# Performance work log

Hardware: AMD Instinct MI355X
Metric: run time of the kernel (lower is better)

## Reference

```python
import jax, jax.numpy as jnp
import numpy as np

B, NPQ, NPV, NSL, K, ED, H = 64, 1024, 256, 1, 128, 16, 8
DK = K // H  # per-head dim (k_dim = v_dim = emb_dim // num_heads)
ETYPES = [("PQ","PQ"),("PQ","PV"),("PQ","Slack"),("PV","PQ"),("PV","PV"),("PV","Slack"),("Slack","PQ"),("Slack","PV")]
ECOUNTS = [262144, 131072, 4096, 131072, 65536, 2048, 4096, 2048]
NN = {"PQ": B*NPQ, "PV": B*NPV, "Slack": B*NSL}
LN_EPS = 1e-5


def setup_inputs() -> dict:
    ks = iter(jax.random.split(jax.random.key(0), 64))
    inp = {}
    for name, n in [("x_PQ", NN["PQ"]), ("x_PV", NN["PV"]), ("x_Slack", NN["Slack"])]:
        inp[name] = jax.random.normal(next(ks), (n, K), jnp.float32)
    for t, ((s, d), E) in enumerate(zip(ETYPES, ECOUNTS)):
        src = jax.random.randint(next(ks), (E,), 0, NN[s])
        dst = jax.random.randint(next(ks), (E,), 0, NN[d])
        inp[f"ei_{t}"] = jnp.stack([src, dst]).astype(jnp.int32)
        inp[f"ea_{t}"] = jax.random.normal(next(ks), (E, ED), jnp.float32)
    sc = 1.0 / np.sqrt(K)
    shapes = {"Wk": (2,8,K,K), "bk": (2,8,K), "Wq": (2,8,K,K), "bq": (2,8,K),
              "Wv": (2,8,K,K), "bv": (2,8,K), "Ws": (2,8,K,K), "bconv": (2,8,K),
              "We": (2,8,ED,K), "be": (2,8,K), "Wgt": (K,K), "bgt": (K,),
              "Wq1": (K,K), "Wk2": (K,K), "Wv2": (K,K), "Wo": (K,K), "bo": (K,)}
    for name, sh in shapes.items():
        inp[name] = jax.random.normal(next(ks), sh, jnp.float32) * sc
    inp["ln_g"] = jnp.ones((K,), jnp.float32)
    inp["ln_b"] = jnp.zeros((K,), jnp.float32)
    return inp


def _cross_attention(x1, x2, Wq1, Wk2, Wv2, Wo, bo):
    # x1: [B, N1, K] queries; x2: [B, N2, K] keys/values
    Bq, N1, _ = x1.shape
    N2 = x2.shape[1]
    q = (x1 @ Wq1).reshape(Bq, N1, H, DK)
    k = (x2 @ Wk2).reshape(Bq, N2, H, DK)
    v = (x2 @ Wv2).reshape(Bq, N2, H, DK)
    attn = jnp.einsum("bnhd,bmhd->bhnm", q, k) / np.sqrt(DK).astype(np.float32)
    attn = jax.nn.softmax(attn, axis=-1)
    out = jnp.einsum("bhnm,bmhd->bnhd", attn, v).reshape(Bq, N1, H * DK)
    return out @ Wo + bo


def _forward(x_PQ, x_PV, x_Slack, ei, ea,
             Wk, bk, Wq, bq, Wv, bv, Ws, bconv, We, be,
             Wgt, bgt, Wq1, Wk2, Wv2, Wo, bo, ln_g, ln_b):
    x = {"PQ": x_PQ, "PV": x_PV, "Slack": x_Slack}
    # global feature from input node features
    gf = jnp.concatenate([x_PQ.reshape(B, NPQ, K),
                          x_PV.reshape(B, NPV, K),
                          x_Slack.reshape(B, NSL, K)], axis=1)
    gf = gf @ Wgt + bgt
    gnode = jnp.concatenate([gf.mean(axis=1, keepdims=True),
                             gf.max(axis=1, keepdims=True)], axis=1)  # [B, 2, K]
    # 2 HeteroConv layers of ResGatedGraphConv, aggr='sum' over edge types
    for l in range(2):
        new = {t: jnp.zeros((NN[t], K), x_PQ.dtype) for t in ("PQ", "PV", "Slack")}
        for t, (s, d) in enumerate(ETYPES):
            xs, xd = x[s], x[d]
            k_ = xd @ Wk[l, t] + bk[l, t]   # lin_key on dst
            q_ = xs @ Wq[l, t] + bq[l, t]   # lin_query on src
            v_ = xs @ Wv[l, t] + bv[l, t]   # lin_value on src
            e_ = ea[t] @ We[l, t] + be[l, t]  # lin_edge
            si, di = ei[t][0], ei[t][1]
            gate = jax.nn.sigmoid(k_[di] + q_[si] + e_)  # [E, K]
            agg = jax.ops.segment_sum(gate * v_[si], di, num_segments=NN[d])
            new[d] = new[d] + agg + xd @ Ws[l, t] + bconv[l, t]
        x = {t: jax.nn.relu(v) for t, v in new.items()}
    # cross-attention vs. global mean/max nodes, residual, layernorm (PQ, PV only)
    res = {}
    for key2, N1 in (("PQ", NPQ), ("PV", NPV)):
        x1 = x[key2].reshape(B, N1, K)
        ca = _cross_attention(x1, gnode, Wq1, Wk2, Wv2, Wo, bo).reshape(B * N1, K)
        h = x[key2] + ca
        mu = h.mean(axis=-1, keepdims=True)
        var = ((h - mu) ** 2).mean(axis=-1, keepdims=True)
        res[key2] = (h - mu) * jax.lax.rsqrt(var + LN_EPS) * ln_g + ln_b
    return res["PQ"], res["PV"], x["Slack"]


def reference(x_PQ, x_PV, x_Slack,
              ei_0, ei_1, ei_2, ei_3, ei_4, ei_5, ei_6, ei_7,
              ea_0, ea_1, ea_2, ea_3, ea_4, ea_5, ea_6, ea_7,
              Wk, bk, Wq, bq, Wv, bv, Ws, bconv, We, be,
              Wgt, bgt, Wq1, Wk2, Wv2, Wo, bo, ln_g, ln_b):
    ei = [ei_0, ei_1, ei_2, ei_3, ei_4, ei_5, ei_6, ei_7]
    ea = [ea_0, ea_1, ea_2, ea_3, ea_4, ea_5, ea_6, ea_7]
    return _forward(x_PQ, x_PV, x_Slack, ei, ea,
                    Wk, bk, Wq, bq, Wv, bv, Ws, bconv, We, be,
                    Wgt, bgt, Wq1, Wk2, Wv2, Wo, bo, ln_g, ln_b)
```

## Files before the change

kernel.cpp:

```cpp
#include <hip/hip_runtime.h>
#include <hip/hip_bf16.h>
#include <math.h>

#define N_PQ 65536
#define N_PV 16384
#define N_SL 64

typedef __attribute__((ext_vector_type(8))) short s16x8;
typedef __attribute__((ext_vector_type(4))) float f32x4;

__device__ __forceinline__ ushort f2bf(float f) {
    union { float f; unsigned u; } x; x.f = f;
    unsigned r = x.u + 0x7fff + ((x.u >> 16) & 1);
    return (ushort)(r >> 16);
}
__device__ __forceinline__ float bf2f(ushort u) {
    union { unsigned u; float f; } x; x.u = ((unsigned)u) << 16;
    return x.f;
}

template<int OUT_BF16>
__global__ __launch_bounds__(256) void gemm_mfma(
    const ushort* __restrict__ A, const ushort* __restrict__ Bt,
    const float* __restrict__ bias, void* __restrict__ Cv, int M, int N)
{
    __shared__ ushort As[128 * 128];
    const int tid = threadIdx.x;
    const int m0 = blockIdx.x * 128;
    const int n0 = blockIdx.y * 128;

    #pragma unroll
    for (int p = 0; p < 8; ++p) {
        int c = p * 256 + tid;
        int row = c >> 4, c16 = c & 15;
        int gr = m0 + row;
        int4 v = make_int4(0, 0, 0, 0);
        if (gr < M) v = *(const int4*)(A + (size_t)gr * 128 + c16 * 8);
        *(int4*)(As + row * 128 + (c16 ^ (row & 7)) * 8) = v;
    }
    __syncthreads();

    const int lane = tid & 63, wave = tid >> 6;
    const int wr = wave >> 1, wc = wave & 1;
    const int lrow = lane & 15, lk = lane >> 4;

    f32x4 acc[4][4];
    #pragma unroll
    for (int mi = 0; mi < 4; ++mi)
        #pragma unroll
        for (int ni = 0; ni < 4; ++ni) acc[mi][ni] = (f32x4){0.f, 0.f, 0.f, 0.f};

    #pragma unroll
    for (int kk = 0; kk < 4; ++kk) {
        s16x8 a[4], b[4];
        #pragma unroll
        for (int mi = 0; mi < 4; ++mi) {
            int row = wr * 64 + mi * 16 + lrow;
            int c16 = (lk + kk * 4) ^ (row & 7);
            a[mi] = *(const s16x8*)(As + row * 128 + c16 * 8);
        }
        #pragma unroll
        for (int ni = 0; ni < 4; ++ni) {
            int n = n0 + wc * 64 + ni * 16 + lrow;
            b[ni] = *(const s16x8*)(Bt + (size_t)n * 128 + kk * 32 + lk * 8);
        }
        #pragma unroll
        for (int mi = 0; mi < 4; ++mi)
            #pragma unroll
            for (int ni = 0; ni < 4; ++ni)
                acc[mi][ni] = __builtin_amdgcn_mfma_f32_16x16x32_bf16(
                    a[mi], b[ni], acc[mi][ni], 0, 0, 0);
    }

    if (OUT_BF16) {
        __syncthreads();
        ushort* Cl = As;
        #pragma unroll
        for (int mi = 0; mi < 4; ++mi)
            #pragma unroll
            for (int ni = 0; ni < 4; ++ni)
                #pragma unroll
                for (int r = 0; r < 4; ++r) {
                    int row = wr * 64 + mi * 16 + (lane >> 4) * 4 + r;
                    int col = wc * 64 + ni * 16 + (lane & 15);
                    float v = acc[mi][ni][r] + (bias ? bias[n0 + col] : 0.f);
                    Cl[row * 128 + (((col >> 3) ^ (row & 7)) << 3) + (col & 7)] = f2bf(v);
                }
        __syncthreads();
        ushort* C = (ushort*)Cv;
        #pragma unroll
        for (int p = 0; p < 8; ++p) {
            int c = p * 256 + tid;
            int row = c >> 4, c16 = c & 15;
            int gr = m0 + row;
            if (gr < M)
                *(int4*)(C + (size_t)gr * N + n0 + c16 * 8) =
                    *(const int4*)(As + row * 128 + (c16 ^ (row & 7)) * 8);
        }
    } else {
        float* C = (float*)Cv;
        #pragma unroll
        for (int mi = 0; mi < 4; ++mi)
            #pragma unroll
            for (int ni = 0; ni < 4; ++ni)
                #pragma unroll
                for (int r = 0; r < 4; ++r) {
                    int row = m0 + wr * 64 + mi * 16 + (lane >> 4) * 4 + r;
                    int col = n0 + wc * 64 + ni * 16 + (lane & 15);
                    if (row < M)
                        C[(size_t)row * N + col] =
                            acc[mi][ni][r] + (bias ? bias[col] : 0.f);
                }
    }
}

__global__ void prep_mats(
    const float* __restrict__ Wk, const float* __restrict__ Wq,
    const float* __restrict__ Wv, const float* __restrict__ Ws,
    const float* __restrict__ Wgt, const float* __restrict__ Wq1,
    const float* __restrict__ Wk2, const float* __restrict__ Wv2,
    const float* __restrict__ Wo,
    ushort* __restrict__ panels, ushort* __restrict__ wssum,
    ushort* __restrict__ finalw)
{
    const int m = blockIdx.x >> 6;
    const int e = (blockIdx.x & 63) * 256 + threadIdx.x;
    const int nl = e >> 7, k = e & 127;
    const int dstlist[3][3] = {{0,3,6},{1,4,7},{2,5,-1}};
    const int srclist[3][3] = {{0,1,2},{3,4,5},{6,7,-1}};
    const int nkg[3] = {3,3,2};
    const int gofs[3] = {0,1280,2560};

    if (m < 52) {
        int l = m / 26, r = m % 26;
        int g, slot;
        if (r < 10)      { g = 0; slot = r; }
        else if (r < 20) { g = 1; slot = r - 10; }
        else             { g = 2; slot = r - 20; }
        int nk = nkg[g];
        float val; int col;
        if (slot < nk) {
            int t = dstlist[g][slot];
            val = Wk[(size_t)(l * 8 + t) * 16384 + k * 128 + nl];
            col = slot * 128 + nl;
        } else if (slot < 2 * nk) {
            int s = slot - nk; int t = srclist[g][s];
            val = Wq[(size_t)(l * 8 + t) * 16384 + k * 128 + nl];
            col = nk * 128 + s * 256 + ((nl >> 1) << 2) + (nl & 1);
        } else if (slot < 3 * nk) {
            int s = slot - 2 * nk; int t = srclist[g][s];
            val = Wv[(size_t)(l * 8 + t) * 16384 + k * 128 + nl];
            col = nk * 128 + s * 256 + ((nl >> 1) << 2) + 2 + (nl & 1);
        } else {
            float s = 0.f;
            #pragma unroll
            for (int i = 0; i < 3; ++i) {
                int t = dstlist[g][i];
                if (t >= 0) s += Ws[(size_t)(l * 8 + t) * 16384 + k * 128 + nl];
            }
            val = s; col = 1152 + nl;
        }
        panels[((size_t)l * 3328 + gofs[g] + col) * 128 + k] = f2bf(val);
    } else if (m < 54) {
        int l = m - 52;
        float s = Ws[(size_t)(l * 8 + 2) * 16384 + k * 128 + nl]
                + Ws[(size_t)(l * 8 + 5) * 16384 + k * 128 + nl];
        wssum[(size_t)l * 16384 + nl * 128 + k] = f2bf(s);
    } else {
        const float* fsrc[5] = {Wgt, Wq1, Wk2, Wv2, Wo};
        int idx = m - 54;
        finalw[(size_t)idx * 16384 + nl * 128 + k] = f2bf(fsrc[idx][k * 128 + nl]);
    }
}

__global__ void prep_bias(
    const float* __restrict__ bk, const float* __restrict__ bq,
    const float* __restrict__ bv, const float* __restrict__ bconv,
    float* __restrict__ bias_cat, float* __restrict__ bcsum)
{
    const int l = blockIdx.x / 3, g = blockIdx.x % 3;
    const int dstlist[3][3] = {{0,3,6},{1,4,7},{2,5,-1}};
    const int srclist[3][3] = {{0,1,2},{3,4,5},{6,7,-1}};
    const int nkg[3] = {3,3,2};
    const int gofs[3] = {0,1280,2560};
    const int nslots = (g < 2) ? 10 : 6;
    int nk = nkg[g];
    for (int idx = threadIdx.x; idx < nslots * 128; idx += 256) {
        int slot = idx >> 7, nl = idx & 127;
        float val; int col;
        if (slot < nk) {
            int t = dstlist[g][slot];
            val = bk[(l * 8 + t) * 128 + nl];
            col = slot * 128 + nl;
        } else if (slot < 2 * nk) {
            int s = slot - nk; int t = srclist[g][s];
            val = bq[(l * 8 + t) * 128 + nl];
            col = nk * 128 + s * 256 + ((nl >> 1) << 2) + (nl & 1);
        } else if (slot < 3 * nk) {
            int s = slot - 2 * nk; int t = srclist[g][s];
            val = bv[(l * 8 + t) * 128 + nl];
            col = nk * 128 + s * 256 + ((nl >> 1) << 2) + 2 + (nl & 1);
        } else {
            float s = 0.f;
            #pragma unroll
            for (int i = 0; i < 3; ++i) {
                int t = dstlist[g][i];
                if (t >= 0) s += bconv[(l * 8 + t) * 128 + nl];
            }
            val = s; col = 1152 + nl;
        }
        bias_cat[l * 3328 + gofs[g] + col] = val;
    }
    if (g == 2 && threadIdx.x < 128) {
        bcsum[l * 128 + threadIdx.x] =
            bconv[(l * 8 + 2) * 128 + threadIdx.x] + bconv[(l * 8 + 5) * 128 + threadIdx.x];
    }
}

struct HArgs {
    const int* ei[6];
    int E[6];
    int base[6];
    int cum[7];
};

__global__ void hist_kernel(HArgs A, int* __restrict__ bins)
{
    int g = blockIdx.x * 256 + threadIdx.x;
    if (g >= A.cum[6]) return;
    int t = 0;
    #pragma unroll
    for (int i = 0; i < 5; ++i) t += (g >= A.cum[i + 1]);
    int e = g - A.cum[t];
    int dst = A.ei[t][A.E[t] + e];
    atomicAdd(&bins[A.base[t] + dst], 1);
}

__global__ __launch_bounds__(256) void scan_a(
    const int* __restrict__ bins, int* __restrict__ offs, int* __restrict__ bsum)
{
    __shared__ int s[256];
    const int b = blockIdx.x, t = threadIdx.x;
    int v = bins[b * 256 + t];
    s[t] = v; __syncthreads();
    #pragma unroll
    for (int off = 1; off < 256; off <<= 1) {
        int x = (t >= off) ? s[t - off] : 0;
        __syncthreads();
        s[t] += x;
        __syncthreads();
    }
    offs[b * 256 + t] = s[t] - v;
    if (t == 255) bsum[b] = s[255];
}

__global__ __launch_bounds__(1024) void scan_b(
    const int* __restrict__ bsum, int* __restrict__ carry)
{
    __shared__ int s[1024];
    const int t = threadIdx.x;
    int v = bsum[t];
    s[t] = v; __syncthreads();
    for (int off = 1; off < 1024; off <<= 1) {
        int x = (t >= off) ? s[t - off] : 0;
        __syncthreads();
        s[t] += x;
        __syncthreads();
    }
    carry[t] = s[t] - v;
}

__global__ void scan_c(int* __restrict__ offs, const int* __restrict__ carry,
                       int* __restrict__ cursor)
{
    const int b = blockIdx.x, t = threadIdx.x;
    int v = offs[b * 256 + t] + carry[b];
    offs[b * 256 + t] = v;
    cursor[b * 256 + t] = v;
}

__global__ void scatter_kernel(HArgs A, int* __restrict__ cursor,
                               int* __restrict__ lsrc, int* __restrict__ leid)
{
    int g = blockIdx.x * 256 + threadIdx.x;
    if (g >= A.cum[6]) return;
    int t = 0;
    #pragma unroll
    for (int i = 0; i < 5; ++i) t += (g >= A.cum[i + 1]);
    int e = g - A.cum[t];
    int src = A.ei[t][e];
    int dst = A.ei[t][A.E[t] + e];
    int pos = atomicAdd(&cursor[A.base[t] + dst], 1);
    lsrc[pos] = src;
    leid[pos] = e;
}

struct GTA {
    int base, kcol, qvcol, lds;
    const ushort* Ys;
    const float* ea;
    const float* We;
    const float* be;
};
struct GArgs {
    GTA t[3];
    const int* offs;
    const int* lsrc;
    const int* leid;
    ushort* xbg;
    const ushort* Yg;
    int ldg, wscol;
};

__global__ __launch_bounds__(256) void gather_kernel(GArgs A)
{
    const int wave = threadIdx.x >> 6, lane = threadIdx.x & 63;
    const int d = blockIdx.x * 4 + wave;
    const int j0 = lane * 2;

    ushort2 w2 = *(const ushort2*)(A.Yg + (size_t)d * A.ldg + A.wscol + j0);
    float a0 = bf2f(w2.x), a1 = bf2f(w2.y);

    #pragma unroll
    for (int i = 0; i < 3; ++i) {
        const GTA T = A.t[i];
        int start = __builtin_amdgcn_readfirstlane(A.offs[T.base + d]);
        int end   = __builtin_amdgcn_readfirstlane(A.offs[T.base + d + 1]);
        if (start == end) continue;

        ushort2 kk = *(const ushort2*)(A.Yg + (size_t)d * A.ldg + T.kcol + j0);
        float k0 = bf2f(kk.x), k1 = bf2f(kk.y);
        float we0[16], we1[16];
        #pragma unroll
        for (int r = 0; r < 16; ++r) {
            float2 wv = *(const float2*)(T.We + r * 128 + j0);
            we0[r] = wv.x; we1[r] = wv.y;
        }
        float2 be2 = *(const float2*)(T.be + j0);

        int eB = (start + 1 < end) ? start + 1 : start;
        int siA  = __builtin_amdgcn_readfirstlane(A.lsrc[start]);
        int eidA = __builtin_amdgcn_readfirstlane(A.leid[start]);
        uint2 qvA = *(const uint2*)(T.Ys + (size_t)siA * T.lds + T.qvcol + lane * 4);
        float4 aA0 = *(const float4*)(T.ea + (size_t)eidA * 16);
        float4 aA1 = *(const float4*)(T.ea + (size_t)eidA * 16 + 4);
        float4 aA2 = *(const float4*)(T.ea + (size_t)eidA * 16 + 8);
        float4 aA3 = *(const float4*)(T.ea + (size_t)eidA * 16 + 12);
        int siB  = __builtin_amdgcn_readfirstlane(A.lsrc[eB]);
        int eidB = __builtin_amdgcn_readfirstlane(A.leid[eB]);
        uint2 qvB = *(const uint2*)(T.Ys + (size_t)siB * T.lds + T.qvcol + lane * 4);
        float4 aB0 = *(const float4*)(T.ea + (size_t)eidB * 16);
        float4 aB1 = *(const float4*)(T.ea + (size_t)eidB * 16 + 4);
        float4 aB2 = *(const float4*)(T.ea + (size_t)eidB * 16 + 8);
        float4 aB3 = *(const float4*)(T.ea + (size_t)eidB * 16 + 12);

        #define COMPUTE(QV, C0, C1, C2, C3) { \
            float e0 = be2.x, e1 = be2.y; \
            e0 += (C0).x*we0[0] + (C0).y*we0[1] + (C0).z*we0[2] + (C0).w*we0[3] \
                + (C1).x*we0[4] + (C1).y*we0[5] + (C1).z*we0[6] + (C1).w*we0[7] \
                + (C2).x*we0[8] + (C2).y*we0[9] + (C2).z*we0[10] + (C2).w*we0[11] \
                + (C3).x*we0[12] + (C3).y*we0[13] + (C3).z*we0[14] + (C3).w*we0[15]; \
            e1 += (C0).x*we1[0] + (C0).y*we1[1] + (C0).z*we1[2] + (C0).w*we1[3] \
                + (C1).x*we1[4] + (C1).y*we1[5] + (C1).z*we1[6] + (C1).w*we1[7] \
                + (C2).x*we1[8] + (C2).y*we1[9] + (C2).z*we1[10] + (C2).w*we1[11] \
                + (C3).x*we1[12] + (C3).y*we1[13] + (C3).z*we1[14] + (C3).w*we1[15]; \
            float q0 = bf2f((ushort)((QV).x & 0xffff)), q1 = bf2f((ushort)((QV).x >> 16)); \
            float v0 = bf2f((ushort)((QV).y & 0xffff)), v1 = bf2f((ushort)((QV).y >> 16)); \
            float g0 = 1.f / (1.f + __expf(-(k0 + q0 + e0))); \
            float g1 = 1.f / (1.f + __expf(-(k1 + q1 + e1))); \
            a0 = fmaf(g0, v0, a0); \
            a1 = fmaf(g1, v1, a1); }

        for (int e = start; e < end; e += 2) {
            uint2 qc = qvA;
            float4 c0 = aA0, c1 = aA1, c2 = aA2, c3 = aA3;
            int nxA = (e + 2 < end) ? e + 2 : e;
            siA  = __builtin_amdgcn_readfirstlane(A.lsrc[nxA]);
            eidA = __builtin_amdgcn_readfirstlane(A.leid[nxA]);
            qvA = *(const uint2*)(T.Ys + (size_t)siA * T.lds + T.qvcol + lane * 4);
            aA0 = *(const float4*)(T.ea + (size_t)eidA * 16);
            aA1 = *(const float4*)(T.ea + (size_t)eidA * 16 + 4);
            aA2 = *(const float4*)(T.ea + (size_t)eidA * 16 + 8);
            aA3 = *(const float4*)(T.ea + (size_t)eidA * 16 + 12);
            COMPUTE(qc, c0, c1, c2, c3)

            if (e + 1 < end) {
                uint2 qc2 = qvB;
                float4 d0 = aB0, d1 = aB1, d2 = aB2, d3 = aB3;
                int nxB = (e + 3 < end) ? e + 3 : e;
                siB  = __builtin_amdgcn_readfirstlane(A.lsrc[nxB]);
                eidB = __builtin_amdgcn_readfirstlane(A.leid[nxB]);
                qvB = *(const uint2*)(T.Ys + (size_t)siB * T.lds + T.qvcol + lane * 4);
                aB0 = *(const float4*)(T.ea + (size_t)eidB * 16);
                aB1 = *(const float4*)(T.ea + (size_t)eidB * 16 + 4);
                aB2 = *(const float4*)(T.ea + (size_t)eidB * 16 + 8);
                aB3 = *(const float4*)(T.ea + (size_t)eidB * 16 + 12);
                COMPUTE(qc2, d0, d1, d2, d3)
            }
        }
        #undef COMPUTE
    }
    ushort2 o; o.x = f2bf(fmaxf(a0, 0.f)); o.y = f2bf(fmaxf(a1, 0.f));
    *(ushort2*)(A.xbg + (size_t)d * 128 + j0) = o;
}

__global__ __launch_bounds__(256) void edge_slack(
    const int* __restrict__ ei, const float* __restrict__ ea,
    const float* __restrict__ We, const float* __restrict__ be,
    const ushort* __restrict__ Yk, int ldk,
    const ushort* __restrict__ Yqv, int ldq,
    float* __restrict__ nd, int E)
{
    const int e = blockIdx.x * 2 + (threadIdx.x >> 7);
    if (e >= E) return;
    const int j = threadIdx.x & 127;
    const int si = ei[e];
    const int di = ei[E + e];

    float ej = be[j];
    #pragma unroll
    for (int r = 0; r < 16; ++r)
        ej += ea[(size_t)e * 16 + r] * We[r * 128 + j];

    float kv = bf2f(Yk[(size_t)di * ldk + j]);
    float qv = bf2f(Yqv[(size_t)si * ldq + ((j >> 1) << 2) + (j & 1)]);
    float vv = bf2f(Yqv[(size_t)si * ldq + ((j >> 1) << 2) + 2 + (j & 1)]);
    float g  = 1.f / (1.f + __expf(-(kv + qv + ej)));
    atomicAdd(&nd[(size_t)di * 128 + j], g * vv);
}

__global__ void f2b_kernel(const float* __restrict__ a, ushort* __restrict__ o, int n)
{
    int i = (blockIdx.x * 256 + threadIdx.x) * 4;
    if (i < n) {
        float4 v = *(const float4*)(a + i);
        ushort4 u; u.x = f2bf(v.x); u.y = f2bf(v.y); u.z = f2bf(v.z); u.w = f2bf(v.w);
        *(ushort4*)(o + i) = u;
    }
}
__global__ void relu_b_kernel(const float* __restrict__ a, ushort* __restrict__ o, int n)
{
    int i = (blockIdx.x * 256 + threadIdx.x) * 4;
    if (i < n) {
        float4 v = *(const float4*)(a + i);
        ushort4 u;
        u.x = f2bf(fmaxf(v.x, 0.f)); u.y = f2bf(fmaxf(v.y, 0.f));
        u.z = f2bf(fmaxf(v.z, 0.f)); u.w = f2bf(fmaxf(v.w, 0.f));
        *(ushort4*)(o + i) = u;
    }
}
__global__ void b2f_kernel(const ushort* __restrict__ a, float* __restrict__ o, int n)
{
    int i = blockIdx.x * 256 + threadIdx.x;
    if (i < n) o[i] = bf2f(a[i]);
}

__global__ void pool1(const ushort* __restrict__ gf, float* __restrict__ pbuf)
{
    const int b = blockIdx.x >> 4, c = blockIdx.x & 15;
    const int j = threadIdx.x;
    float s = 0.f, m = -INFINITY;
    const ushort* pq = gf + (size_t)(b * 1024 + c * 64) * 128;
    for (int i = 0; i < 64; ++i) { float v = bf2f(pq[i * 128 + j]); s += v; m = fmaxf(m, v); }
    const ushort* pv = gf + (size_t)(N_PQ + b * 256 + c * 16) * 128;
    for (int i = 0; i < 16; ++i) { float v = bf2f(pv[i * 128 + j]); s += v; m = fmaxf(m, v); }
    if (c == 0) { float v = bf2f(gf[(size_t)(N_PQ + N_PV + b) * 128 + j]); s += v; m = fmaxf(m, v); }
    pbuf[(size_t)blockIdx.x * 256 + j] = s;
    pbuf[(size_t)blockIdx.x * 256 + 128 + j] = m;
}
__global__ void pool2(const float* __restrict__ pbuf, float* __restrict__ gnode)
{
    const int b = blockIdx.x, j = threadIdx.x;
    float s = 0.f, m = -INFINITY;
    for (int c = 0; c < 16; ++c) {
        s += pbuf[(size_t)(b * 16 + c) * 256 + j];
        m = fmaxf(m, pbuf[(size_t)(b * 16 + c) * 256 + 128 + j]);
    }
    gnode[(size_t)(b * 2) * 128 + j]     = s * (1.f / 1281.f);
    gnode[(size_t)(b * 2 + 1) * 128 + j] = m;
}

__global__ __launch_bounds__(256) void attn_kernel(
    const ushort* __restrict__ q, const float* __restrict__ k2,
    const float* __restrict__ v2, ushort* __restrict__ ao, int shift, int Ntot)
{
    const int n = blockIdx.x * 2 + (threadIdx.x >> 7);
    if (n >= Ntot) return;
    const int j = threadIdx.x & 127;
    const int b = n >> shift;
    const int h16 = j & ~15;

    const ushort* qn = q + (size_t)n * 128 + h16;
    const float* k0 = k2 + (size_t)(b * 2) * 128 + h16;
    const float* k1 = k2 + (size_t)(b * 2 + 1) * 128 + h16;
    float s0 = 0.f, s1 = 0.f;
    #pragma unroll
    for (int d = 0; d < 16; ++d) {
        float qq = bf2f(qn[d]); s0 += qq * k0[d]; s1 += qq * k1[d];
    }
    s0 *= 0.25f; s1 *= 0.25f;
    float m  = fmaxf(s0, s1);
    float a0 = __expf(s0 - m), a1 = __expf(s1 - m);
    float inv = 1.f / (a0 + a1);
    ao[(size_t)n * 128 + j] = f2bf(
        (a0 * v2[(size_t)(b * 2) * 128 + j] + a1 * v2[(size_t)(b * 2 + 1) * 128 + j]) * inv);
}

__global__ __launch_bounds__(256) void ln_kernel(
    const ushort* __restrict__ x, const float* __restrict__ ca,
    const float* __restrict__ g, const float* __restrict__ bb,
    float* __restrict__ out, int N)
{
    const int n = blockIdx.x * 4 + (threadIdx.x >> 6);
    if (n >= N) return;
    const int l = threadIdx.x & 63;
    const size_t base = (size_t)n * 128;
    float h0 = bf2f(x[base + l * 2])     + ca[base + l * 2];
    float h1 = bf2f(x[base + l * 2 + 1]) + ca[base + l * 2 + 1];
    float s  = h0 + h1;
    float ss = h0 * h0 + h1 * h1;
    #pragma unroll
    for (int o = 32; o; o >>= 1) { s += __shfl_xor(s, o); ss += __shfl_xor(ss, o); }
    float mu  = s * (1.f / 128.f);
    float var = ss * (1.f / 128.f) - mu * mu;
    float rs  = rsqrtf(var + 1e-5f);
    out[base + l * 2]     = (h0 - mu) * rs * g[l * 2]     + bb[l * 2];
    out[base + l * 2 + 1] = (h1 - mu) * rs * g[l * 2 + 1] + bb[l * 2 + 1];
}

extern "C" void kernel_launch(void* const* d_in, const int* in_sizes, int n_in,
                              void* d_out, int out_size, void* d_ws, size_t ws_size,
                              hipStream_t stream)
{
    const float* xin[3] = {(const float*)d_in[0], (const float*)d_in[1], (const float*)d_in[2]};
    const int NNs[3] = {N_PQ, N_PV, N_SL};
    const int ncol[3] = {1280, 1280, 768};
    const int gofs[3] = {0, 1280, 2560};

    const int*   ei[8];
    const float* ea[8];
    int          Ecnt[8];
    for (int t = 0; t < 8; ++t) {
        ei[t]   = (const int*)d_in[3 + 2 * t];
        ea[t]   = (const float*)d_in[4 + 2 * t];
        Ecnt[t] = in_sizes[3 + 2 * t] / 2;
    }
    const float* Wk    = (const float*)d_in[19];
    const float* bk    = (const float*)d_in[20];
    const float* Wq    = (const float*)d_in[21];
    const float* bq    = (const float*)d_in[22];
    const float* Wv    = (const float*)d_in[23];
    const float* bv    = (const float*)d_in[24];
    const float* Ws    = (const float*)d_in[25];
    const float* bconv = (const float*)d_in[26];
    const float* We    = (const float*)d_in[27];
    const float* be    = (const float*)d_in[28];
    const float* Wgt   = (const float*)d_in[29];
    const float* bgt   = (const float*)d_in[30];
    const float* Wq1   = (const float*)d_in[31];
    const float* Wk2   = (const float*)d_in[32];
    const float* Wv2   = (const float*)d_in[33];
    const float* Wo    = (const float*)d_in[34];
    const float* bo    = (const float*)d_in[35];
    const float* ln_g  = (const float*)d_in[36];
    const float* ln_b  = (const float*)d_in[37];

    char* w = (char*)d_ws;
    ushort* Y[3];
    Y[0] = (ushort*)w; w += (size_t)N_PQ * 1280 * 2;
    Y[1] = (ushort*)w; w += (size_t)N_PV * 1280 * 2;
    Y[2] = (ushort*)w; w += (size_t)N_SL * 768 * 2;
    ushort* xb[3];
    xb[0] = (ushort*)w; w += (size_t)N_PQ * 128 * 2;
    xb[1] = (ushort*)w; w += (size_t)N_PV * 128 * 2;
    xb[2] = (ushort*)w; w += (size_t)N_SL * 128 * 2;
    ushort* panels = (ushort*)w; w += (size_t)2 * 3328 * 128 * 2;
    ushort* wssum  = (ushort*)w; w += (size_t)2 * 16384 * 2;
    ushort* finalw = (ushort*)w; w += (size_t)5 * 16384 * 2;
    float* bias_cat = (float*)w; w += 6656 * 4;
    float* bcsum    = (float*)w; w += 256 * 4;
    float* gnode    = (float*)w; w += 16384 * 4;
    ushort* gnodeb  = (ushort*)w; w += 16384 * 2;
    float* k2       = (float*)w; w += 16384 * 4;
    float* v2       = (float*)w; w += 16384 * 4;
    float* pbuf     = (float*)w; w += 1024 * 256 * 4;
    const int NBINS = 262144;
    int* bins   = (int*)w; w += (size_t)NBINS * 4;
    int* offs   = (int*)w; w += (size_t)NBINS * 4;
    int* cursor = (int*)w; w += (size_t)NBINS * 4;
    int* bsum   = (int*)w; w += 1024 * 4;
    int* carry  = (int*)w; w += 1024 * 4;
    int* lsrc   = (int*)w; w += (size_t)600064 * 4;
    int* leid   = (int*)w; w += (size_t)600064 * 4;
    ushort* gf   = Y[0];
    ushort* qb   = Y[0];
    ushort* ao   = Y[0] + (size_t)81920 * 128;
    float*  cbuf = (float*)(Y[0] + (size_t)2 * 81920 * 128);
    float* outp = (float*)d_out;
    float* nw2 = outp + (size_t)(N_PQ + N_PV) * 128;

    const ushort* Wgt_t = finalw;
    const ushort* Wq1_t = finalw + 16384;
    const ushort* Wk2_t = finalw + 32768;
    const ushort* Wv2_t = finalw + 49152;
    const ushort* Wo_t  = finalw + 65536;

    auto gemm_b = [&](const ushort* A, const ushort* Bt, const float* bias,
                      ushort* C, int M, int N) {
        gemm_mfma<1><<<dim3((M + 127) / 128, N / 128), 256, 0, stream>>>(A, Bt, bias, C, M, N);
    };
    auto gemm_f = [&](const ushort* A, const ushort* Bt, const float* bias,
                      float* C, int M, int N) {
        gemm_mfma<0><<<dim3((M + 127) / 128, N / 128), 256, 0, stream>>>(A, Bt, bias, C, M, N);
    };

    prep_mats<<<59 * 64, 256, 0, stream>>>(Wk, Wq, Wv, Ws, Wgt, Wq1, Wk2, Wv2, Wo,
                                           panels, wssum, finalw);
    prep_bias<<<6, 256, 0, stream>>>(bk, bq, bv, bconv, bias_cat, bcsum);
    for (int g = 0; g < 3; ++g) {
        int n = NNs[g] * 128;
        f2b_kernel<<<dim3((n / 4 + 255) / 256), 256, 0, stream>>>(xin[g], xb[g], n);
    }

    const int csr_t[6]    = {0, 3, 6, 1, 4, 7};
    const int csr_base[6] = {0, 65536, 131072, 196608, 212992, 229376};
    HArgs ha;
    {
        int c = 0;
        for (int i = 0; i < 6; ++i) {
            int t = csr_t[i];
            ha.ei[i] = ei[t]; ha.E[i] = Ecnt[t]; ha.base[i] = csr_base[i];
            ha.cum[i] = c; c += Ecnt[t];
        }
        ha.cum[6] = c;
    }
    hipMemsetAsync(bins, 0, (size_t)NBINS * 4, stream);
    hist_kernel<<<dim3((ha.cum[6] + 255) / 256), 256, 0, stream>>>(ha, bins);
    scan_a<<<1024, 256, 0, stream>>>(bins, offs, bsum);
    scan_b<<<1, 1024, 0, stream>>>(bsum, carry);
    scan_c<<<1024, 256, 0, stream>>>(offs, carry, cursor);
    scatter_kernel<<<dim3((ha.cum[6] + 255) / 256), 256, 0, stream>>>(ha, cursor, lsrc, leid);

    gemm_b(xb[0], Wgt_t, bgt, gf, N_PQ + N_PV + N_SL, 128);
    pool1<<<1024, 128, 0, stream>>>(gf, pbuf);
    pool2<<<64, 128, 0, stream>>>(pbuf, gnode);
    f2b_kernel<<<dim3(16384 / 4 / 256), 256, 0, stream>>>(gnode, gnodeb, 16384);
    gemm_f(gnodeb, Wk2_t, nullptr, k2, 128, 128);
    gemm_f(gnodeb, Wv2_t, nullptr, v2, 128, 128);

    for (int l = 0; l < 2; ++l) {
        for (int g = 0; g < 3; ++g)
            gemm_b(xb[g], panels + ((size_t)l * 3328 + gofs[g]) * 128,
                   bias_cat + l * 3328 + gofs[g], Y[g], NNs[g], ncol[g]);
        gemm_f(xb[2], wssum + (size_t)l * 16384, bcsum + l * 128, nw2, N_SL, 128);

        for (int g = 0; g < 2; ++g) {
            GArgs ga;
            for (int i = 0; i < 3; ++i) {
                int t = csr_t[g * 3 + i], off = l * 8 + t;
                int sgrp = (i == 2) ? 2 : i;
                ga.t[i].base  = csr_base[g * 3 + i];
                ga.t[i].kcol  = i * 128;
                ga.t[i].lds   = ncol[sgrp];
                ga.t[i].qvcol = ((sgrp == 2) ? 256 : 384) + g * 256;
                ga.t[i].Ys    = Y[sgrp];
                ga.t[i].ea    = ea[t];
                ga.t[i].We    = We + (size_t)off * 2048;
                ga.t[i].be    = be + (size_t)off * 128;
            }
            ga.offs = offs; ga.lsrc = lsrc; ga.leid = leid;
            ga.xbg = xb[g]; ga.Yg = Y[g]; ga.ldg = ncol[g]; ga.wscol = 1152;
            gather_kernel<<<dim3(NNs[g] / 4), 256, 0, stream>>>(ga);
        }

        {
            int off2 = l * 8 + 2;
            edge_slack<<<dim3((Ecnt[2] + 1) / 2), 256, 0, stream>>>(
                ei[2], ea[2], We + (size_t)off2 * 2048, be + (size_t)off2 * 128,
                Y[2] + 0, 768, Y[0] + 896, 1280, nw2, Ecnt[2]);
            int off5 = l * 8 + 5;
            edge_slack<<<dim3((Ecnt[5] + 1) / 2), 256, 0, stream>>>(
                ei[5], ea[5], We + (size_t)off5 * 2048, be + (size_t)off5 * 128,
                Y[2] + 128, 768, Y[1] + 896, 1280, nw2, Ecnt[5]);
        }
        relu_b_kernel<<<dim3(8), 256, 0, stream>>>(nw2, xb[2], N_SL * 128);
    }

    gemm_b(xb[0], Wq1_t, nullptr, qb, N_PQ + N_PV, 128);
    attn_kernel<<<dim3(N_PQ / 2), 256, 0, stream>>>(qb, k2, v2, ao, 10, N_PQ);
    attn_kernel<<<dim3(N_PV / 2), 256, 0, stream>>>(qb + (size_t)N_PQ * 128, k2, v2,
                                                    ao + (size_t)N_PQ * 128, 8, N_PV);
    gemm_f(ao, Wo_t, bo, cbuf, N_PQ + N_PV, 128);
    ln_kernel<<<dim3((N_PQ + N_PV) / 4), 256, 0, stream>>>(xb[0], cbuf, ln_g, ln_b,
                                                           outp, N_PQ + N_PV);
    b2f_kernel<<<dim3((N_SL * 128 + 255) / 256), 256, 0, stream>>>(
        xb[2], outp + (size_t)(N_PQ + N_PV) * 128, N_SL * 128);
}
```

Measured before the change: 910.8 us.

## Reuse staged A tile across two N panels per GEMM block; bf16 cross-attn output

The bf16-output GEMM now loops over two 128-column panels per block when N is a multiple of 256, so the A tile staged into shared memory once is reused for both panels. The bf16 epilogue goes through a separate half-size shared buffer, written in two halves with extra barriers. The output projection of the cross-attention now writes bf16 instead of fp32, and the layernorm reads it as bf16, which halves that intermediate's traffic at some precision cost. Blocks become longer and the grid shrinks, which may lower occupancy and parallelism on the wide GEMMs.

```diff
diff --git a/kernel.cpp b/kernel.cpp
--- a/kernel.cpp
+++ b/kernel.cpp
@@ -19,15 +19,15 @@
     return x.f;
 }
 
-template<int OUT_BF16>
+template<int OUT_BF16, int NPAN>
 __global__ __launch_bounds__(256) void gemm_mfma(
     const ushort* __restrict__ A, const ushort* __restrict__ Bt,
     const float* __restrict__ bias, void* __restrict__ Cv, int M, int N)
 {
     __shared__ ushort As[128 * 128];
+    __shared__ ushort Cs[OUT_BF16 ? 64 * 128 : 64];
     const int tid = threadIdx.x;
     const int m0 = blockIdx.x * 128;
-    const int n0 = blockIdx.y * 128;
 
     #pragma unroll
     for (int p = 0; p < 8; ++p) {
@@ -44,73 +44,82 @@
     const int wr = wave >> 1, wc = wave & 1;
     const int lrow = lane & 15, lk = lane >> 4;
 
-    f32x4 acc[4][4];
-    #pragma unroll
-    for (int mi = 0; mi < 4; ++mi)
-        #pragma unroll
-        for (int ni = 0; ni < 4; ++ni) acc[mi][ni] = (f32x4){0.f, 0.f, 0.f, 0.f};
-
-    #pragma unroll
-    for (int kk = 0; kk < 4; ++kk) {
-        s16x8 a[4], b[4];
-        #pragma unroll
-        for (int mi = 0; mi < 4; ++mi) {
-            int row = wr * 64 + mi * 16 + lrow;
-            int c16 = (lk + kk * 4) ^ (row & 7);
-            a[mi] = *(const s16x8*)(As + row * 128 + c16 * 8);
-        }
-        #pragma unroll
-        for (int ni = 0; ni < 4; ++ni) {
-            int n = n0 + wc * 64 + ni * 16 + lrow;
-            b[ni] = *(const s16x8*)(Bt + (size_t)n * 128 + kk * 32 + lk * 8);
-        }
+    for (int pan = 0; pan < NPAN; ++pan) {
+        const int n0 = (blockIdx.y * NPAN + pan) * 128;
+
+        f32x4 acc[4][4];
         #pragma unroll
         for (int mi = 0; mi < 4; ++mi)
             #pragma unroll
-            for (int ni = 0; ni < 4; ++ni)
-                acc[mi][ni] = __builtin_amdgcn_mfma_f32_16x16x32_bf16(
-                    a[mi], b[ni], acc[mi][ni], 0, 0, 0);
-    }
-
-    if (OUT_BF16) {
-        __syncthreads();
-        ushort* Cl = As;
+            for (int ni = 0; ni < 4; ++ni) acc[mi][ni] = (f32x4){0.f, 0.f, 0.f, 0.f};
+
         #pragma unroll
-        for (int mi = 0; mi < 4; ++mi)
+        for (int kk = 0; kk < 4; ++kk) {
+            s16x8 a[4], b[4];
             #pragma unroll
-            for (int ni = 0; ni < 4; ++ni)
+            for (int mi = 0; mi < 4; ++mi) {
+                int row = wr * 64 + mi * 16 + lrow;
+                int c16 = (lk + kk * 4) ^ (row & 7);
+                a[mi] = *(const s16x8*)(As + row * 128 + c16 * 8);
+            }
+            #pragma unroll
+            for (int ni = 0; ni < 4; ++ni) {
+                int n = n0 + wc * 64 + ni * 16 + lrow;
+                b[ni] = *(const s16x8*)(Bt + (size_t)n * 128 + kk * 32 + lk * 8);
+            }
+            #pragma unroll
+            for (int mi = 0; mi < 4; ++mi)
                 #pragma unroll
-                for (int r = 0; r < 4; ++r) {
-                    int row = wr * 64 + mi * 16 + (lane >> 4) * 4 + r;
-                    int col = wc * 64 + ni * 16 + (lane & 15);
-                    float v = acc[mi][ni][r] + (bias ? bias[n0 + col] : 0.f);
-                    Cl[row * 128 + (((col >> 3) ^ (row & 7)) << 3) + (col & 7)] = f2bf(v);
+                for (int ni = 0; ni < 4; ++ni)
+                    acc[mi][ni] = __builtin_amdgcn_mfma_f32_16x16x32_bf16(
+                        a[mi], b[ni], acc[mi][ni], 0, 0, 0);
+        }
+
+        if (OUT_BF16) {
+            #pragma unroll
+            for (int h = 0; h < 2; ++h) {
+                if (wr == h) {
+                    #pragma unroll
+                    for (int mi = 0; mi < 4; ++mi)
+                        #pragma unroll
+                        for (int ni = 0; ni < 4; ++ni)
+                            #pragma unroll
+                            for (int r = 0; r < 4; ++r) {
+                                int row = mi * 16 + (lane >> 4) * 4 + r;
+                                int col = wc * 64 + ni * 16 + (lane & 15);
+                                float v = acc[mi][ni][r] + (bias ? bias[n0 + col] : 0.f);
+                                Cs[row * 128 + (((col >> 3) ^ (row & 7)) << 3) + (col & 7)]
+                                    = f2bf(v);
+                            }
                 }
-        __syncthreads();
-        ushort* C = (ushort*)Cv;
-        #pragma unroll
-        for (int p = 0; p < 8; ++p) {
-            int c = p * 256 + tid;
-            int row = c >> 4, c16 = c & 15;
-            int gr = m0 + row;
-            if (gr < M)
-                *(int4*)(C + (size_t)gr * N + n0 + c16 * 8) =
-                    *(const int4*)(As + row * 128 + (c16 ^ (row & 7)) * 8);
-        }
-    } else {
-        float* C = (float*)Cv;
-        #pragma unroll
-        for (int mi = 0; mi < 4; ++mi)
+                __syncthreads();
+                ushort* C = (ushort*)Cv;
+                #pragma unroll
+                for (int p2 = 0; p2 < 4; ++p2) {
+                    int c = p2 * 256 + tid;
+                    int row = c >> 4, c16 = c & 15;
+                    int gr = m0 + h * 64 + row;
+                    if (gr < M)
+                        *(int4*)(C + (size_t)gr * N + n0 + c16 * 8) =
+                            *(const int4*)(Cs + row * 128 + (c16 ^ (row & 7)) * 8);
+                }
+                __syncthreads();
+            }
+        } else {
+            float* C = (float*)Cv;
             #pragma unroll
-            for (int ni = 0; ni < 4; ++ni)
+            for (int mi = 0; mi < 4; ++mi)
                 #pragma unroll
-                for (int r = 0; r < 4; ++r) {
-                    int row = m0 + wr * 64 + mi * 16 + (lane >> 4) * 4 + r;
-                    int col = n0 + wc * 64 + ni * 16 + (lane & 15);
-                    if (row < M)
-                        C[(size_t)row * N + col] =
-                            acc[mi][ni][r] + (bias ? bias[col] : 0.f);
-                }
+                for (int ni = 0; ni < 4; ++ni)
+                    #pragma unroll
+                    for (int r = 0; r < 4; ++r) {
+                        int row = m0 + wr * 64 + mi * 16 + (lane >> 4) * 4 + r;
+                        int col = n0 + wc * 64 + ni * 16 + (lane & 15);
+                        if (row < M)
+                            C[(size_t)row * N + col] =
+                                acc[mi][ni][r] + (bias ? bias[col] : 0.f);
+                    }
+        }
     }
 }
 
@@ -507,7 +516,7 @@
 }
 
 __global__ __launch_bounds__(256) void ln_kernel(
-    const ushort* __restrict__ x, const float* __restrict__ ca,
+    const ushort* __restrict__ x, const ushort* __restrict__ ca,
     const float* __restrict__ g, const float* __restrict__ bb,
     float* __restrict__ out, int N)
 {
@@ -515,8 +524,8 @@
     if (n >= N) return;
     const int l = threadIdx.x & 63;
     const size_t base = (size_t)n * 128;
-    float h0 = bf2f(x[base + l * 2])     + ca[base + l * 2];
-    float h1 = bf2f(x[base + l * 2 + 1]) + ca[base + l * 2 + 1];
+    float h0 = bf2f(x[base + l * 2])     + bf2f(ca[base + l * 2]);
+    float h1 = bf2f(x[base + l * 2 + 1]) + bf2f(ca[base + l * 2 + 1]);
     float s  = h0 + h1;
     float ss = h0 * h0 + h1 * h1;
     #pragma unroll
@@ -592,10 +601,10 @@
     int* carry  = (int*)w; w += 1024 * 4;
     int* lsrc   = (int*)w; w += (size_t)600064 * 4;
     int* leid   = (int*)w; w += (size_t)600064 * 4;
-    ushort* gf   = Y[0];
-    ushort* qb   = Y[0];
-    ushort* ao   = Y[0] + (size_t)81920 * 128;
-    float*  cbuf = (float*)(Y[0] + (size_t)2 * 81920 * 128);
+    ushort* gf    = Y[0];
+    ushort* qb    = Y[0];
+    ushort* ao    = Y[0] + (size_t)81920 * 128;
+    ushort* cbufb = Y[0] + (size_t)2 * 81920 * 128;
     float* outp = (float*)d_out;
     float* nw2 = outp + (size_t)(N_PQ + N_PV) * 128;
 
@@ -607,11 +616,17 @@
 
     auto gemm_b = [&](const ushort* A, const ushort* Bt, const float* bias,
                       ushort* C, int M, int N) {
-        gemm_mfma<1><<<dim3((M + 127) / 128, N / 128), 256, 0, stream>>>(A, Bt, bias, C, M, N);
+        if (N % 256 == 0)
+            gemm_mfma<1, 2><<<dim3((M + 127) / 128, N / 256), 256, 0, stream>>>(
+                A, Bt, bias, C, M, N);
+        else
+            gemm_mfma<1, 1><<<dim3((M + 127) / 128, N / 128), 256, 0, stream>>>(
+                A, Bt, bias, C, M, N);
     };
     auto gemm_f = [&](const ushort* A, const ushort* Bt, const float* bias,
                       float* C, int M, int N) {
-        gemm_mfma<0><<<dim3((M + 127) / 128, N / 128), 256, 0, stream>>>(A, Bt, bias, C, M, N);
+        gemm_mfma<0, 1><<<dim3((M + 127) / 128, N / 128), 256, 0, stream>>>(
+            A, Bt, bias, C, M, N);
     };
 
     prep_mats<<<59 * 64, 256, 0, stream>>>(Wk, Wq, Wv, Ws, Wgt, Wq1, Wk2, Wv2, Wo,
@@ -690,8 +705,8 @@
     attn_kernel<<<dim3(N_PQ / 2), 256, 0, stream>>>(qb, k2, v2, ao, 10, N_PQ);
     attn_kernel<<<dim3(N_PV / 2), 256, 0, stream>>>(qb + (size_t)N_PQ * 128, k2, v2,
                                                     ao + (size_t)N_PQ * 128, 8, N_PV);
-    gemm_f(ao, Wo_t, bo, cbuf, N_PQ + N_PV, 128);
-    ln_kernel<<<dim3((N_PQ + N_PV) / 4), 256, 0, stream>>>(xb[0], cbuf, ln_g, ln_b,
+    gemm_b(ao, Wo_t, bo, cbufb, N_PQ + N_PV, 128);
+    ln_kernel<<<dim3((N_PQ + N_PV) / 4), 256, 0, stream>>>(xb[0], cbufb, ln_g, ln_b,
                                                            outp, N_PQ + N_PV);
     b2f_kernel<<<dim3((N_SL * 128 + 255) / 256), 256, 0, stream>>>(
         xb[2], outp + (size_t)(N_PQ + N_PV) * 128, N_SL * 128);
```

Measured after the change: 1.130 ms. 24.1% more time.
